# Optimization experiments

Measured on AMD Instinct MI355X. Metric: run time of the kernel, lower is better.

Reference implementation:

```python
import jax, jax.numpy as jnp
import numpy as np

HIDDEN = 1024
HEADS = 8
HEAD_DIM = HIDDEN // HEADS  # 128
MAX_SEQ = 4096
MAX_TOKS = 2048
THETA = 10000.0
INIT_STD = 0.02


def setup_inputs() -> dict:
    key = jax.random.key(0)
    ks = jax.random.split(key, 8)
    B, L = 2, 4096
    hidden_states = jax.random.normal(ks[0], (B, L, HIDDEN), dtype=jnp.float32)
    attention_mask = jnp.ones((B, L), dtype=bool)
    segment_ids = jnp.sort(jax.random.randint(ks[1], (B, L), 0, 2), axis=-1).astype(jnp.int32)
    position_ids = jnp.sort(jax.random.randint(ks[2], (B, L), 0, MAX_SEQ), axis=-1).astype(jnp.int32)
    # nn.Linear weights stored (out_features, in_features), bias=False, normal(0, 0.02)
    wq = (jax.random.normal(ks[3], (HIDDEN, HIDDEN), dtype=jnp.float32) * INIT_STD)
    wk = (jax.random.normal(ks[4], (HIDDEN, HIDDEN), dtype=jnp.float32) * INIT_STD)
    wv = (jax.random.normal(ks[5], (HIDDEN, HIDDEN), dtype=jnp.float32) * INIT_STD)
    wo = (jax.random.normal(ks[6], (HIDDEN, HIDDEN), dtype=jnp.float32) * INIT_STD)
    return {
        "hidden_states": hidden_states,
        "wq": wq, "wk": wk, "wv": wv, "wo": wo,
        "attention_mask": attention_mask,
        "segment_ids": segment_ids,
        "position_ids": position_ids,
    }


def _freqs_cis(position_ids):
    # precompute_freqs_cis gathered at position_ids -> (B, L, HEAD_DIM//2) complex
    inv_freq = 1.0 / (THETA ** (jnp.arange(0, HEAD_DIM, 2, dtype=jnp.float32) / HEAD_DIM))
    ang = position_ids.astype(jnp.float32)[..., None] * inv_freq  # (B,L,D/2)
    return jax.lax.complex(jnp.cos(ang), jnp.sin(ang))


def _apply_rope(x, fc):
    # x: (B,L,H,D); fc: (B,L,D/2) complex; broadcast fc over heads
    xs = x.astype(jnp.float32).reshape(*x.shape[:-1], HEAD_DIM // 2, 2)
    xc = jax.lax.complex(xs[..., 0], xs[..., 1])  # (B,L,H,D/2)
    out = xc * fc[:, :, None, :]
    return jnp.stack([jnp.real(out), jnp.imag(out)], axis=-1).reshape(x.shape).astype(x.dtype)


def reference(hidden_states, wq, wk, wv, wo, attention_mask, segment_ids, position_ids):
    B, L, _ = hidden_states.shape
    q = (hidden_states @ wq.T).reshape(B, L, HEADS, HEAD_DIM)
    k = (hidden_states @ wk.T).reshape(B, L, HEADS, HEAD_DIM)
    v = (hidden_states @ wv.T).reshape(B, L, HEADS, HEAD_DIM)

    fc = _freqs_cis(position_ids)
    q = _apply_rope(q, fc)
    k = _apply_rope(k, fc)

    # block-causal mask: query block index >= key block index
    blk = jnp.arange(L) // MAX_TOKS
    causal = blk[:, None] >= blk[None, :]                                   # (L,L)
    seg = (segment_ids[:, :, None] == segment_ids[:, None, :])              # (B,L,L)
    mask = attention_mask[:, None, None, :] & seg[:, None, :, :] & causal[None, None, :, :]

    scale = 1.0 / np.float32(np.sqrt(HEAD_DIM))
    scores = jnp.einsum('bqhd,bkhd->bhqk', q, k) * scale                    # (B,H,L,L)
    scores = jnp.where(mask, scores, jnp.float32(-jnp.inf))
    probs = jax.nn.softmax(scores, axis=-1)
    attn = jnp.einsum('bhqk,bkhd->bqhd', probs, v).reshape(B, L, HIDDEN)
    return attn @ wo.T
```

## Files before the change

### kernel.cpp

```cpp
#include <hip/hip_runtime.h>
#include <hip/hip_bf16.h>
#include <cstdint>
#include <cstddef>
#include <type_traits>

#define HID 1024
#define HEADS 8
#define HDIM 128
#define SEQ 4096
#define BATCH 2

typedef float f32x4 __attribute__((ext_vector_type(4)));
typedef float f32x16 __attribute__((ext_vector_type(16)));
typedef short bf16x8 __attribute__((ext_vector_type(8)));
typedef unsigned short u16x8 __attribute__((ext_vector_type(8)));

typedef bf16x8 __attribute__((may_alias)) bf16x8_a;
typedef u16x8  __attribute__((may_alias)) u16x8_a;
typedef float4 __attribute__((may_alias)) float4_a;
typedef unsigned int __attribute__((may_alias)) u32_a;

__device__ __forceinline__ unsigned short f2bf(float f) {
    union { float f; unsigned int u; } v; v.f = f;
    unsigned int u = v.u;
    unsigned int r = (u + 0x7FFFu + ((u >> 16) & 1u)) >> 16;
    return (unsigned short)r;
}
__device__ __forceinline__ float bf2f(unsigned short h) {
    union { unsigned int u; float f; } v; v.u = ((unsigned int)h) << 16;
    return v.f;
}

__device__ __forceinline__ void plane_swap(unsigned int& x, unsigned int& y) {
    asm("v_permlane32_swap_b32 %0, %1" : "+v"(x), "+v"(y));
}
__device__ __forceinline__ unsigned int cvt_pk(float lo, float hi) {
    unsigned int r;
    asm("v_cvt_pk_bf16_f32 %0, %1, %2" : "=v"(r) : "v"(lo), "v"(hi));
    return r;
}
__device__ __forceinline__ bf16x8 pack4(unsigned int a, unsigned int b,
                                        unsigned int c, unsigned int d) {
    union { unsigned int u[4]; bf16x8 v; } t;
    t.u[0] = a; t.u[1] = b; t.u[2] = c; t.u[3] = d;
    return t.v;
}
__device__ __forceinline__ void g2lds16(const unsigned short* g, unsigned short* l) {
    __builtin_amdgcn_global_load_lds(
        (const __attribute__((address_space(1))) void*)g,
        (__attribute__((address_space(3))) void*)l, 16, 0, 0);
}

__global__ __launch_bounds__(256)
void cvt_kernel(const float* __restrict__ X, unsigned short* __restrict__ Y)
{
    int i = (blockIdx.x * 256 + threadIdx.x) * 8;
    float4 d0 = *(const float4_a*)&X[i];
    float4 d1 = *(const float4_a*)&X[i + 4];
    u16x8 t;
    t[0] = f2bf(d0.x); t[1] = f2bf(d0.y); t[2] = f2bf(d0.z); t[3] = f2bf(d0.w);
    t[4] = f2bf(d1.x); t[5] = f2bf(d1.y); t[6] = f2bf(d1.z); t[7] = f2bf(d1.w);
    *(u16x8_a*)&Y[i] = t;
}

__global__ __launch_bounds__(256)
void cvtw_kernel(const float* __restrict__ w0, const float* __restrict__ w1,
                 const float* __restrict__ w2, const float* __restrict__ w3,
                 unsigned short* __restrict__ Y)
{
    const int WSZ8 = (HID * HID) / 8;
    int c = blockIdx.x * 256 + threadIdx.x;
    int quarter = c >> 17;
    int idx = (c & (WSZ8 - 1)) * 8;
    const float* w = quarter == 0 ? w0 : quarter == 1 ? w1 : quarter == 2 ? w2 : w3;
    float4 d0 = *(const float4_a*)&w[idx];
    float4 d1 = *(const float4_a*)&w[idx + 4];
    u16x8 t;
    t[0] = f2bf(d0.x); t[1] = f2bf(d0.y); t[2] = f2bf(d0.z); t[3] = f2bf(d0.w);
    t[4] = f2bf(d1.x); t[5] = f2bf(d1.y); t[6] = f2bf(d1.z); t[7] = f2bf(d1.w);
    *(u16x8_a*)&Y[(size_t)quarter * HID * HID + idx] = t;
}

template<typename OutT>
__global__ __launch_bounds__(256)
void gemm_swz(const unsigned short* __restrict__ A, const unsigned short* __restrict__ B,
              OutT* __restrict__ C, int M, int N, int K, int lda)
{
    __shared__ __align__(16) unsigned short Al[128][64];
    __shared__ __align__(16) unsigned short Bl[128][64];
    const int tid  = threadIdx.x;
    const int lane = tid & 63;
    const int w    = tid >> 6;
    const int wr   = w >> 1, wc = w & 1;
    const int l16  = lane & 15, l4 = lane >> 4;
    const int tm   = blockIdx.y * 128, tn = blockIdx.x * 128;
    const int srow  = lane >> 3;
    const int sslot = (lane & 7) ^ srow;

    f32x4 acc[4][4] = {};

    for (int ko = 0; ko < K; ko += 64) {
        __syncthreads();
#pragma unroll
        for (int it = 0; it < 4; ++it) {
            int ca = w * 4 + it;
            int row = ca * 8 + srow;
            g2lds16(&A[(size_t)(tm + row) * lda + ko + sslot * 8], &Al[ca * 8][0]);
            g2lds16(&B[(size_t)(tn + row) * K   + ko + sslot * 8], &Bl[ca * 8][0]);
        }
        __syncthreads();
#pragma unroll
        for (int kk = 0; kk < 2; ++kk) {
            const int rslot = (kk * 4 + l4) ^ (l16 & 7);
            bf16x8 af[4], bfr[4];
#pragma unroll
            for (int i = 0; i < 4; ++i)
                af[i] = *(const bf16x8_a*)&Al[wr*64 + i*16 + l16][rslot * 8];
#pragma unroll
            for (int j = 0; j < 4; ++j)
                bfr[j] = *(const bf16x8_a*)&Bl[wc*64 + j*16 + l16][rslot * 8];
#pragma unroll
            for (int i = 0; i < 4; ++i)
#pragma unroll
                for (int j = 0; j < 4; ++j)
                    acc[i][j] = __builtin_amdgcn_mfma_f32_16x16x32_bf16(af[i], bfr[j], acc[i][j], 0, 0, 0);
        }
    }
#pragma unroll
    for (int i = 0; i < 4; ++i)
#pragma unroll
        for (int j = 0; j < 4; ++j)
#pragma unroll
            for (int r = 0; r < 4; ++r) {
                int row = tm + wr*64 + i*16 + l4*4 + r;
                int col = tn + wc*64 + j*16 + l16;
                if constexpr (std::is_same<OutT, float>::value)
                    C[(size_t)row * N + col] = acc[i][j][r];
                else
                    C[(size_t)row * N + col] = f2bf(acc[i][j][r]);
            }
}

template<bool A_BF16, bool B_BF16, typename OutT>
__global__ __launch_bounds__(256)
void gemm_bt(const void* __restrict__ Av, const void* __restrict__ Bv,
             OutT* __restrict__ C, int M, int N, int K, int lda)
{
    __shared__ __align__(16) unsigned short Al[128][72];
    __shared__ __align__(16) unsigned short Bl[128][72];
    const int tid  = threadIdx.x;
    const int lane = tid & 63;
    const int w    = tid >> 6;
    const int wr   = w >> 1, wc = w & 1;
    const int l16  = lane & 15, l4 = lane >> 4;
    const int tm   = blockIdx.y * 128, tn = blockIdx.x * 128;

    f32x4 acc[4][4] = {};

    for (int ko = 0; ko < K; ko += 64) {
        __syncthreads();
#pragma unroll
        for (int it = 0; it < 4; ++it) {
            int c = tid + 256 * it;
            int row = c >> 3, col0 = (c & 7) * 8;
            if constexpr (A_BF16) {
                const unsigned short* A = (const unsigned short*)Av;
                *(u16x8_a*)&Al[row][col0] =
                    *(const u16x8_a*)&A[(size_t)(tm + row) * lda + ko + col0];
            } else {
                const float* A = (const float*)Av;
                const float* p = &A[(size_t)(tm + row) * lda + ko + col0];
                float4 d0 = *(const float4_a*)p;
                float4 d1 = *(const float4_a*)(p + 4);
                u16x8 t;
                t[0] = f2bf(d0.x); t[1] = f2bf(d0.y); t[2] = f2bf(d0.z); t[3] = f2bf(d0.w);
                t[4] = f2bf(d1.x); t[5] = f2bf(d1.y); t[6] = f2bf(d1.z); t[7] = f2bf(d1.w);
                *(u16x8_a*)&Al[row][col0] = t;
            }
            if constexpr (B_BF16) {
                const unsigned short* B = (const unsigned short*)Bv;
                *(u16x8_a*)&Bl[row][col0] =
                    *(const u16x8_a*)&B[(size_t)(tn + row) * K + ko + col0];
            } else {
                const float* B = (const float*)Bv;
                const float* p = &B[(size_t)(tn + row) * K + ko + col0];
                float4 d0 = *(const float4_a*)p;
                float4 d1 = *(const float4_a*)(p + 4);
                u16x8 t;
                t[0] = f2bf(d0.x); t[1] = f2bf(d0.y); t[2] = f2bf(d0.z); t[3] = f2bf(d0.w);
                t[4] = f2bf(d1.x); t[5] = f2bf(d1.y); t[6] = f2bf(d1.z); t[7] = f2bf(d1.w);
                *(u16x8_a*)&Bl[row][col0] = t;
            }
        }
        __syncthreads();
#pragma unroll
        for (int kk = 0; kk < 2; ++kk) {
            bf16x8 af[4], bfr[4];
#pragma unroll
            for (int i = 0; i < 4; ++i)
                af[i] = *(const bf16x8_a*)&Al[wr*64 + i*16 + l16][kk*32 + l4*8];
#pragma unroll
            for (int j = 0; j < 4; ++j)
                bfr[j] = *(const bf16x8_a*)&Bl[wc*64 + j*16 + l16][kk*32 + l4*8];
#pragma unroll
            for (int i = 0; i < 4; ++i)
#pragma unroll
                for (int j = 0; j < 4; ++j)
                    acc[i][j] = __builtin_amdgcn_mfma_f32_16x16x32_bf16(af[i], bfr[j], acc[i][j], 0, 0, 0);
        }
    }
#pragma unroll
    for (int i = 0; i < 4; ++i)
#pragma unroll
        for (int j = 0; j < 4; ++j)
#pragma unroll
            for (int r = 0; r < 4; ++r) {
                int row = tm + wr*64 + i*16 + l4*4 + r;
                int col = tn + wc*64 + j*16 + l16;
                if constexpr (std::is_same<OutT, float>::value)
                    C[(size_t)row * N + col] = acc[i][j][r];
                else
                    C[(size_t)row * N + col] = f2bf(acc[i][j][r]);
            }
}

template<int HSH>
__global__ __launch_bounds__(256)
void rope_kernel(unsigned short* __restrict__ X, const int* __restrict__ pos_ids, int RS)
{
    int c = blockIdx.x * 256 + threadIdx.x;
    int d0 = (c & 15) * 8;
    int h  = (c >> 4) & ((1 << HSH) - 1);
    int l  = (c >> (4 + HSH)) & 4095;
    int b  = c >> (16 + HSH);
    int pos = pos_ids[b * SEQ + l];
    size_t off = (size_t)(b * SEQ + l) * RS + h * HDIM + d0;
    u16x8 d = *(const u16x8_a*)&X[off];
    float x[8];
#pragma unroll
    for (int j = 0; j < 8; ++j) x[j] = bf2f(d[j]);
#pragma unroll
    for (int j = 0; j < 4; ++j) {
        int i = (d0 >> 1) + j;
        float invf = powf(10000.0f, -(float)i * (1.0f / 64.0f));
        float ang = (float)pos * invf;
        float s, cth;
        sincosf(ang, &s, &cth);
        float o0 = x[2*j] * cth - x[2*j+1] * s;
        float o1 = x[2*j] * s   + x[2*j+1] * cth;
        d[2*j]   = f2bf(o0);
        d[2*j+1] = f2bf(o1);
    }
    *(u16x8_a*)&X[off] = d;
}

__global__ __launch_bounds__(256, 2)
void attn_kernel(const unsigned short* Q,
                 const unsigned short* K,
                 const unsigned short* V,
                 const int* __restrict__ seg,
                 unsigned short* O, int RS)
{
    __shared__ __align__(16) unsigned short Kl[64][136];
    __shared__ __align__(16) unsigned short Vt[128][72];

    const int tid  = threadIdx.x;
    const int lane = tid & 63;
    const int l32  = lane & 31, hi = lane >> 5;
    const int w    = tid >> 6;
    const int qt = (SEQ / 128 - 1) - blockIdx.x;
    const int h  = blockIdx.y;
    const int b  = blockIdx.z;
    const int qg0 = qt * 128 + w * 32;
    const int hoff = h * HDIM;

    bf16x8 qf[8];
    {
        size_t base = (size_t)(b * SEQ + qg0 + l32) * RS + hoff;
#pragma unroll
        for (int kk = 0; kk < 8; ++kk)
            qf[kk] = *(const bf16x8_a*)&Q[base + kk*16 + hi*8];
    }

    f32x16 acco0 = {}, acco1 = {}, acco2 = {}, acco3 = {};
    float lsum = 0.f;

    const int nkt = ((qt >> 4) + 1) * 32;

    int lo = 0, hb = SEQ;
    while (lo < hb) { int mid = (lo + hb) >> 1; if (seg[b * SEQ + mid] == 0) lo = mid + 1; else hb = mid; }
    const int boundary = lo;
    const bool blk_seg1 = (seg[b * SEQ + qt * 128] == 1);
    const bool blk_seg0 = (seg[b * SEQ + qt * 128 + 127] == 0);
    const bool mixed = !blk_seg0 && !blk_seg1;
    int kstart = 0, kend = nkt;
    if (blk_seg1) kstart = boundary >> 6;
    if (blk_seg0) {
        int ke = (boundary + 63) >> 6;
        kend = ke < nkt ? ke : nkt;
    }
    const bool qlt = (qg0 + l32) < boundary;

    const int kp = tid & 31, db = tid >> 5;
    const float sc = 0.08838834764831845f;

    u16x8 kreg[4], v0a, v0b, v1a, v1b;
    {
        const int kb = kstart * 64;
#pragma unroll
        for (int it = 0; it < 4; ++it) {
            int c = tid + 256 * it;
            kreg[it] = *(const u16x8_a*)&K[(size_t)(b * SEQ + kb + (c >> 4)) * RS + hoff + (c & 15) * 8];
        }
        size_t vb0 = (size_t)(b * SEQ + kb + 2 * kp) * RS + hoff + db * 16;
        size_t vb1 = (size_t)(b * SEQ + kb + 2 * kp + 1) * RS + hoff + db * 16;
        v0a = *(const u16x8_a*)&V[vb0];     v0b = *(const u16x8_a*)&V[vb0 + 8];
        v1a = *(const u16x8_a*)&V[vb1];     v1b = *(const u16x8_a*)&V[vb1 + 8];
    }

    for (int kt = kstart; kt < kend; ++kt) {
        const int kb = kt * 64;
        __syncthreads();
#pragma unroll
        for (int it = 0; it < 4; ++it) {
            int c = tid + 256 * it;
            *(u16x8_a*)&Kl[c >> 4][(c & 15) * 8] = kreg[it];
        }
#pragma unroll
        for (int j = 0; j < 8; ++j) {
            *(u32_a*)&Vt[db * 16 + j][2 * kp] =
                (unsigned int)(unsigned short)v0a[j] | ((unsigned int)(unsigned short)v1a[j] << 16);
            *(u32_a*)&Vt[db * 16 + 8 + j][2 * kp] =
                (unsigned int)(unsigned short)v0b[j] | ((unsigned int)(unsigned short)v1b[j] << 16);
        }
        __syncthreads();

        if (kt + 1 < kend) {
            const int kb2 = (kt + 1) * 64;
#pragma unroll
            for (int it = 0; it < 4; ++it) {
                int c = tid + 256 * it;
                kreg[it] = *(const u16x8_a*)&K[(size_t)(b * SEQ + kb2 + (c >> 4)) * RS + hoff + (c & 15) * 8];
            }
            size_t vb0 = (size_t)(b * SEQ + kb2 + 2 * kp) * RS + hoff + db * 16;
            size_t vb1 = (size_t)(b * SEQ + kb2 + 2 * kp + 1) * RS + hoff + db * 16;
            v0a = *(const u16x8_a*)&V[vb0];     v0b = *(const u16x8_a*)&V[vb0 + 8];
            v1a = *(const u16x8_a*)&V[vb1];     v1b = *(const u16x8_a*)&V[vb1 + 8];
        }

        f32x16 a0 = {}, a1 = {};
#pragma unroll
        for (int kk = 0; kk < 8; ++kk) {
            bf16x8 k0 = *(const bf16x8_a*)&Kl[     l32][kk*16 + hi*8];
            bf16x8 k1 = *(const bf16x8_a*)&Kl[32 + l32][kk*16 + hi*8];
            a0 = __builtin_amdgcn_mfma_f32_32x32x16_bf16(k0, qf[kk], a0, 0, 0, 0);
            a1 = __builtin_amdgcn_mfma_f32_32x32x16_bf16(k1, qf[kk], a1, 0, 0, 0);
        }

        unsigned int pk0[8], pk1[8];
        const bool need_mask = mixed || (kb < boundary && kb + 64 > boundary);
        if (need_mask) {
            const int kb0 = kb + 4 * hi, kb1 = kb + 32 + 4 * hi;
#pragma unroll
            for (int i = 0; i < 8; ++i) {
                int r0 = 2 * i;
                int off = (r0 & 3) + 8 * (r0 >> 2);
                float p0 = ((kb0 + off     < boundary) == qlt) ? __expf(a0[r0]     * sc) : 0.0f;
                float p1 = ((kb0 + off + 1 < boundary) == qlt) ? __expf(a0[r0 + 1] * sc) : 0.0f;
                float q0 = ((kb1 + off     < boundary) == qlt) ? __expf(a1[r0]     * sc) : 0.0f;
                float q1 = ((kb1 + off + 1 < boundary) == qlt) ? __expf(a1[r0 + 1] * sc) : 0.0f;
                lsum += (p0 + p1) + (q0 + q1);
                pk0[i] = cvt_pk(p0, p1);
                pk1[i] = cvt_pk(q0, q1);
            }
        } else {
#pragma unroll
            for (int i = 0; i < 8; ++i) {
                int r0 = 2 * i;
                float p0 = __expf(a0[r0]     * sc);
                float p1 = __expf(a0[r0 + 1] * sc);
                float q0 = __expf(a1[r0]     * sc);
                float q1 = __expf(a1[r0 + 1] * sc);
                lsum += (p0 + p1) + (q0 + q1);
                pk0[i] = cvt_pk(p0, p1);
                pk1[i] = cvt_pk(q0, q1);
            }
        }
        plane_swap(pk0[0], pk0[2]); plane_swap(pk0[1], pk0[3]);
        plane_swap(pk0[4], pk0[6]); plane_swap(pk0[5], pk0[7]);
        plane_swap(pk1[0], pk1[2]); plane_swap(pk1[1], pk1[3]);
        plane_swap(pk1[4], pk1[6]); plane_swap(pk1[5], pk1[7]);
        bf16x8 pf[4];
        pf[0] = pack4(pk0[0], pk0[1], pk0[2], pk0[3]);
        pf[1] = pack4(pk0[4], pk0[5], pk0[6], pk0[7]);
        pf[2] = pack4(pk1[0], pk1[1], pk1[2], pk1[3]);
        pf[3] = pack4(pk1[4], pk1[5], pk1[6], pk1[7]);

#pragma unroll
        for (int ks = 0; ks < 4; ++ks) {
            bf16x8 vf0 = *(const bf16x8_a*)&Vt[      l32][ks*16 + hi*8];
            bf16x8 vf1 = *(const bf16x8_a*)&Vt[32  + l32][ks*16 + hi*8];
            bf16x8 vf2 = *(const bf16x8_a*)&Vt[64  + l32][ks*16 + hi*8];
            bf16x8 vf3 = *(const bf16x8_a*)&Vt[96  + l32][ks*16 + hi*8];
            acco0 = __builtin_amdgcn_mfma_f32_32x32x16_bf16(pf[ks], vf0, acco0, 0, 0, 0);
            acco1 = __builtin_amdgcn_mfma_f32_32x32x16_bf16(pf[ks], vf1, acco1, 0, 0, 0);
            acco2 = __builtin_amdgcn_mfma_f32_32x32x16_bf16(pf[ks], vf2, acco2, 0, 0, 0);
            acco3 = __builtin_amdgcn_mfma_f32_32x32x16_bf16(pf[ks], vf3, acco3, 0, 0, 0);
        }
    }

    float tot = lsum + __shfl_xor(lsum, 32, 64);
#pragma unroll
    for (int r = 0; r < 16; ++r) {
        int qrow = (r & 3) + 8 * (r >> 2) + 4 * hi;
        float inv = 1.0f / __shfl(tot, qrow, 64);
        size_t base = (size_t)(b * SEQ + qg0 + qrow) * RS + hoff;
        O[base +       l32] = f2bf(acco0[r] * inv);
        O[base +  32 + l32] = f2bf(acco1[r] * inv);
        O[base +  64 + l32] = f2bf(acco2[r] * inv);
        O[base +  96 + l32] = f2bf(acco3[r] * inv);
    }
}

extern "C" void kernel_launch(void* const* d_in, const int* in_sizes, int n_in,
                              void* d_out, int out_size, void* d_ws, size_t ws_size,
                              hipStream_t stream)
{
    const float* X  = (const float*)d_in[0];
    const float* wq = (const float*)d_in[1];
    const float* wk = (const float*)d_in[2];
    const float* wv = (const float*)d_in[3];
    const float* wo = (const float*)d_in[4];
    const int* seg = (const int*)d_in[n_in - 2];
    const int* pos = (const int*)d_in[n_in - 1];
    float* out = (float*)d_out;

    const size_t NTOK = (size_t)BATCH * SEQ;
    const size_t MAT  = NTOK * HID;
    const size_t WSZ  = (size_t)HID * HID;

    if (ws_size >= (4 * MAT + 4 * WSZ) * sizeof(unsigned short)) {
        unsigned short* QKVb = (unsigned short*)d_ws;
        unsigned short* Xb   = QKVb + 3 * MAT;
        unsigned short* Wb   = Xb + MAT;
        unsigned short* Wob  = Wb + 3 * WSZ;

        cvt_kernel<<<(int)(MAT / (256 * 8)), 256, 0, stream>>>(X, Xb);
        cvtw_kernel<<<(int)(4 * WSZ / (256 * 8)), 256, 0, stream>>>(wq, wk, wv, wo, Wb);

        dim3 gq(3 * HID / 128, (int)(NTOK / 128));
        gemm_swz<unsigned short><<<gq, 256, 0, stream>>>(
            Xb, Wb, QKVb, (int)NTOK, 3 * HID, HID, HID);

        rope_kernel<4><<<(BATCH * SEQ * 16 * 16) / 256, 256, 0, stream>>>(QKVb, pos, 3 * HID);

        dim3 ga(SEQ / 128, HEADS, BATCH);
        attn_kernel<<<ga, 256, 0, stream>>>(QKVb, QKVb + HID, QKVb + 2 * HID, seg,
                                            QKVb , 3 * HID);

        dim3 go(HID / 128, (int)(NTOK / 128));
        gemm_swz<float><<<go, 256, 0, stream>>>(
            QKVb, Wob, out, (int)NTOK, HID, HID, 3 * HID);
    } else {
        unsigned short* Qb = (unsigned short*)d_ws;
        unsigned short* Kb = Qb + MAT;
        unsigned short* Vb = Kb + MAT;

        dim3 gg(HID / 128, (int)(NTOK / 128));
        gemm_bt<false, false, unsigned short><<<gg, 256, 0, stream>>>(
            (const void*)X, (const void*)wq, Qb, (int)NTOK, HID, HID, HID);
        gemm_bt<false, false, unsigned short><<<gg, 256, 0, stream>>>(
            (const void*)X, (const void*)wk, Kb, (int)NTOK, HID, HID, HID);
        gemm_bt<false, false, unsigned short><<<gg, 256, 0, stream>>>(
            (const void*)X, (const void*)wv, Vb, (int)NTOK, HID, HID, HID);

        rope_kernel<3><<<(BATCH * SEQ * HEADS * 16) / 256, 256, 0, stream>>>(Qb, pos, HID);
        rope_kernel<3><<<(BATCH * SEQ * HEADS * 16) / 256, 256, 0, stream>>>(Kb, pos, HID);

        dim3 ga(SEQ / 128, HEADS, BATCH);
        attn_kernel<<<ga, 256, 0, stream>>>(Qb, Kb, Vb, seg, Qb, HID);

        gemm_bt<true, false, float><<<gg, 256, 0, stream>>>(
            (const void*)Qb, (const void*)wo, out, (int)NTOK, HID, HID, HID);
    }
}
```

Measured before the change: 229.2 us.

## Double-buffer attention K/V shared tiles and amortize RoPE sincos across heads

The attention kernel now keeps two LDS buffers for the K and V tiles. The next tile is written into the alternate buffer after the PV MMAs, which needs only one barrier per iteration instead of two. Separately, the RoPE kernel computes sin/cos once per token and dimension chunk and reuses them across all 16 (or 8) head slices, so far fewer transcendental evaluations and threads are needed. The cost is doubled LDS use per block, which may affect occupancy, and fewer, longer RoPE threads.

```diff
diff --git a/kernel.cpp b/kernel.cpp
--- a/kernel.cpp
+++ b/kernel.cpp
@@ -224,34 +224,35 @@
             }
 }
 
-template<int HSH>
+template<int NH>
 __global__ __launch_bounds__(256)
 void rope_kernel(unsigned short* __restrict__ X, const int* __restrict__ pos_ids, int RS)
 {
     int c = blockIdx.x * 256 + threadIdx.x;
     int d0 = (c & 15) * 8;
-    int h  = (c >> 4) & ((1 << HSH) - 1);
-    int l  = (c >> (4 + HSH)) & 4095;
-    int b  = c >> (16 + HSH);
+    int l  = (c >> 4) & 4095;
+    int b  = c >> 16;
     int pos = pos_ids[b * SEQ + l];
-    size_t off = (size_t)(b * SEQ + l) * RS + h * HDIM + d0;
-    u16x8 d = *(const u16x8_a*)&X[off];
-    float x[8];
-#pragma unroll
-    for (int j = 0; j < 8; ++j) x[j] = bf2f(d[j]);
+    float sth[4], cth[4];
 #pragma unroll
     for (int j = 0; j < 4; ++j) {
         int i = (d0 >> 1) + j;
         float invf = powf(10000.0f, -(float)i * (1.0f / 64.0f));
         float ang = (float)pos * invf;
-        float s, cth;
-        sincosf(ang, &s, &cth);
-        float o0 = x[2*j] * cth - x[2*j+1] * s;
-        float o1 = x[2*j] * s   + x[2*j+1] * cth;
-        d[2*j]   = f2bf(o0);
-        d[2*j+1] = f2bf(o1);
-    }
-    *(u16x8_a*)&X[off] = d;
+        sincosf(ang, &sth[j], &cth[j]);
+    }
+    size_t base = (size_t)(b * SEQ + l) * RS + d0;
+#pragma unroll
+    for (int h = 0; h < NH; ++h) {
+        u16x8 d = *(const u16x8_a*)&X[base + h * HDIM];
+#pragma unroll
+        for (int j = 0; j < 4; ++j) {
+            float x0 = bf2f(d[2*j]), x1 = bf2f(d[2*j+1]);
+            d[2*j]   = f2bf(x0 * cth[j] - x1 * sth[j]);
+            d[2*j+1] = f2bf(x0 * sth[j] + x1 * cth[j]);
+        }
+        *(u16x8_a*)&X[base + h * HDIM] = d;
+    }
 }
 
 __global__ __launch_bounds__(256, 2)
@@ -261,8 +262,8 @@
                  const int* __restrict__ seg,
                  unsigned short* O, int RS)
 {
-    __shared__ __align__(16) unsigned short Kl[64][136];
-    __shared__ __align__(16) unsigned short Vt[128][72];
+    __shared__ __align__(16) unsigned short Kl[2][64][136];
+    __shared__ __align__(16) unsigned short Vt[2][128][72];
 
     const int tid  = threadIdx.x;
     const int lane = tid & 63;
@@ -317,42 +318,41 @@
         v0a = *(const u16x8_a*)&V[vb0];     v0b = *(const u16x8_a*)&V[vb0 + 8];
         v1a = *(const u16x8_a*)&V[vb1];     v1b = *(const u16x8_a*)&V[vb1 + 8];
     }
-
+#pragma unroll
+    for (int it = 0; it < 4; ++it) {
+        int c = tid + 256 * it;
+        *(u16x8_a*)&Kl[0][c >> 4][(c & 15) * 8] = kreg[it];
+    }
+#pragma unroll
+    for (int j = 0; j < 8; ++j) {
+        *(u32_a*)&Vt[0][db * 16 + j][2 * kp] =
+            (unsigned int)(unsigned short)v0a[j] | ((unsigned int)(unsigned short)v1a[j] << 16);
+        *(u32_a*)&Vt[0][db * 16 + 8 + j][2 * kp] =
+            (unsigned int)(unsigned short)v0b[j] | ((unsigned int)(unsigned short)v1b[j] << 16);
+    }
+    if (kstart + 1 < kend) {
+        const int kb2 = (kstart + 1) * 64;
+#pragma unroll
+        for (int it = 0; it < 4; ++it) {
+            int c = tid + 256 * it;
+            kreg[it] = *(const u16x8_a*)&K[(size_t)(b * SEQ + kb2 + (c >> 4)) * RS + hoff + (c & 15) * 8];
+        }
+        size_t vb0 = (size_t)(b * SEQ + kb2 + 2 * kp) * RS + hoff + db * 16;
+        size_t vb1 = (size_t)(b * SEQ + kb2 + 2 * kp + 1) * RS + hoff + db * 16;
+        v0a = *(const u16x8_a*)&V[vb0];     v0b = *(const u16x8_a*)&V[vb0 + 8];
+        v1a = *(const u16x8_a*)&V[vb1];     v1b = *(const u16x8_a*)&V[vb1 + 8];
+    }
+    __syncthreads();
+
+    int buf = 0;
     for (int kt = kstart; kt < kend; ++kt) {
         const int kb = kt * 64;
-        __syncthreads();
-#pragma unroll
-        for (int it = 0; it < 4; ++it) {
-            int c = tid + 256 * it;
-            *(u16x8_a*)&Kl[c >> 4][(c & 15) * 8] = kreg[it];
-        }
-#pragma unroll
-        for (int j = 0; j < 8; ++j) {
-            *(u32_a*)&Vt[db * 16 + j][2 * kp] =
-                (unsigned int)(unsigned short)v0a[j] | ((unsigned int)(unsigned short)v1a[j] << 16);
-            *(u32_a*)&Vt[db * 16 + 8 + j][2 * kp] =
-                (unsigned int)(unsigned short)v0b[j] | ((unsigned int)(unsigned short)v1b[j] << 16);
-        }
-        __syncthreads();
-
-        if (kt + 1 < kend) {
-            const int kb2 = (kt + 1) * 64;
-#pragma unroll
-            for (int it = 0; it < 4; ++it) {
-                int c = tid + 256 * it;
-                kreg[it] = *(const u16x8_a*)&K[(size_t)(b * SEQ + kb2 + (c >> 4)) * RS + hoff + (c & 15) * 8];
-            }
-            size_t vb0 = (size_t)(b * SEQ + kb2 + 2 * kp) * RS + hoff + db * 16;
-            size_t vb1 = (size_t)(b * SEQ + kb2 + 2 * kp + 1) * RS + hoff + db * 16;
-            v0a = *(const u16x8_a*)&V[vb0];     v0b = *(const u16x8_a*)&V[vb0 + 8];
-            v1a = *(const u16x8_a*)&V[vb1];     v1b = *(const u16x8_a*)&V[vb1 + 8];
-        }
 
         f32x16 a0 = {}, a1 = {};
 #pragma unroll
         for (int kk = 0; kk < 8; ++kk) {
-            bf16x8 k0 = *(const bf16x8_a*)&Kl[     l32][kk*16 + hi*8];
-            bf16x8 k1 = *(const bf16x8_a*)&Kl[32 + l32][kk*16 + hi*8];
+            bf16x8 k0 = *(const bf16x8_a*)&Kl[buf][     l32][kk*16 + hi*8];
+            bf16x8 k1 = *(const bf16x8_a*)&Kl[buf][32 + l32][kk*16 + hi*8];
             a0 = __builtin_amdgcn_mfma_f32_32x32x16_bf16(k0, qf[kk], a0, 0, 0, 0);
             a1 = __builtin_amdgcn_mfma_f32_32x32x16_bf16(k1, qf[kk], a1, 0, 0, 0);
         }
@@ -398,15 +398,45 @@
 
 #pragma unroll
         for (int ks = 0; ks < 4; ++ks) {
-            bf16x8 vf0 = *(const bf16x8_a*)&Vt[      l32][ks*16 + hi*8];
-            bf16x8 vf1 = *(const bf16x8_a*)&Vt[32  + l32][ks*16 + hi*8];
-            bf16x8 vf2 = *(const bf16x8_a*)&Vt[64  + l32][ks*16 + hi*8];
-            bf16x8 vf3 = *(const bf16x8_a*)&Vt[96  + l32][ks*16 + hi*8];
+            bf16x8 vf0 = *(const bf16x8_a*)&Vt[buf][      l32][ks*16 + hi*8];
+            bf16x8 vf1 = *(const bf16x8_a*)&Vt[buf][32  + l32][ks*16 + hi*8];
+            bf16x8 vf2 = *(const bf16x8_a*)&Vt[buf][64  + l32][ks*16 + hi*8];
+            bf16x8 vf3 = *(const bf16x8_a*)&Vt[buf][96  + l32][ks*16 + hi*8];
             acco0 = __builtin_amdgcn_mfma_f32_32x32x16_bf16(pf[ks], vf0, acco0, 0, 0, 0);
             acco1 = __builtin_amdgcn_mfma_f32_32x32x16_bf16(pf[ks], vf1, acco1, 0, 0, 0);
             acco2 = __builtin_amdgcn_mfma_f32_32x32x16_bf16(pf[ks], vf2, acco2, 0, 0, 0);
             acco3 = __builtin_amdgcn_mfma_f32_32x32x16_bf16(pf[ks], vf3, acco3, 0, 0, 0);
         }
+
+        if (kt + 1 < kend) {
+            const int nb = buf ^ 1;
+#pragma unroll
+            for (int it = 0; it < 4; ++it) {
+                int c = tid + 256 * it;
+                *(u16x8_a*)&Kl[nb][c >> 4][(c & 15) * 8] = kreg[it];
+            }
+#pragma unroll
+            for (int j = 0; j < 8; ++j) {
+                *(u32_a*)&Vt[nb][db * 16 + j][2 * kp] =
+                    (unsigned int)(unsigned short)v0a[j] | ((unsigned int)(unsigned short)v1a[j] << 16);
+                *(u32_a*)&Vt[nb][db * 16 + 8 + j][2 * kp] =
+                    (unsigned int)(unsigned short)v0b[j] | ((unsigned int)(unsigned short)v1b[j] << 16);
+            }
+            if (kt + 2 < kend) {
+                const int kb2 = (kt + 2) * 64;
+#pragma unroll
+                for (int it = 0; it < 4; ++it) {
+                    int c = tid + 256 * it;
+                    kreg[it] = *(const u16x8_a*)&K[(size_t)(b * SEQ + kb2 + (c >> 4)) * RS + hoff + (c & 15) * 8];
+                }
+                size_t vb0 = (size_t)(b * SEQ + kb2 + 2 * kp) * RS + hoff + db * 16;
+                size_t vb1 = (size_t)(b * SEQ + kb2 + 2 * kp + 1) * RS + hoff + db * 16;
+                v0a = *(const u16x8_a*)&V[vb0];     v0b = *(const u16x8_a*)&V[vb0 + 8];
+                v1a = *(const u16x8_a*)&V[vb1];     v1b = *(const u16x8_a*)&V[vb1 + 8];
+            }
+            __syncthreads();
+        }
+        buf ^= 1;
     }
 
     float tot = lsum + __shfl_xor(lsum, 32, 64);
@@ -452,7 +482,7 @@
         gemm_swz<unsigned short><<<gq, 256, 0, stream>>>(
             Xb, Wb, QKVb, (int)NTOK, 3 * HID, HID, HID);
 
-        rope_kernel<4><<<(BATCH * SEQ * 16 * 16) / 256, 256, 0, stream>>>(QKVb, pos, 3 * HID);
+        rope_kernel<16><<<(BATCH * SEQ * 16) / 256, 256, 0, stream>>>(QKVb, pos, 3 * HID);
 
         dim3 ga(SEQ / 128, HEADS, BATCH);
         attn_kernel<<<ga, 256, 0, stream>>>(QKVb, QKVb + HID, QKVb + 2 * HID, seg,
@@ -474,8 +504,8 @@
         gemm_bt<false, false, unsigned short><<<gg, 256, 0, stream>>>(
             (const void*)X, (const void*)wv, Vb, (int)NTOK, HID, HID, HID);
 
-        rope_kernel<3><<<(BATCH * SEQ * HEADS * 16) / 256, 256, 0, stream>>>(Qb, pos, HID);
-        rope_kernel<3><<<(BATCH * SEQ * HEADS * 16) / 256, 256, 0, stream>>>(Kb, pos, HID);
+        rope_kernel<8><<<(BATCH * SEQ * 16) / 256, 256, 0, stream>>>(Qb, pos, HID);
+        rope_kernel<8><<<(BATCH * SEQ * 16) / 256, 256, 0, stream>>>(Kb, pos, HID);
 
         dim3 ga(SEQ / 128, HEADS, BATCH);
         attn_kernel<<<ga, 256, 0, stream>>>(Qb, Kb, Vb, seg, Qb, HID);
```

Result: faster. 204.3 us (-10.9%).
